# Kernel tuning notes

Measured on AMD Instinct MI355X. Metric: run time of the kernel, lower is better.

The kernel has to match this reference:

```python
import jax, jax.numpy as jnp
import numpy as np

DIMS = 1024
FF_DIMS = 4096
EPS = 1e-5


def _ln(x, g, b):
    m = jnp.mean(x, axis=-1, keepdims=True)
    v = jnp.mean(jnp.square(x - m), axis=-1, keepdims=True)
    return (x - m) * jax.lax.rsqrt(v + EPS) * g + b


def _bind(a, b):
    # HRR bind = circular convolution via FFT
    n = b.shape[-1]
    return jnp.fft.irfft(jnp.fft.rfft(a) * jnp.fft.rfft(b), n=n)


def _unbind(s, a):
    # HRR unbind = circular correlation (bind with approximate inverse) = conj in freq
    n = s.shape[-1]
    return jnp.fft.irfft(jnp.fft.rfft(s) * jnp.conj(jnp.fft.rfft(a)), n=n)


def setup_inputs() -> dict:
    key = jax.random.key(0)
    ks = jax.random.split(key, 16)
    d, f = DIMS, FF_DIMS
    s_d = 1.0 / np.sqrt(d)
    s_f = 1.0 / np.sqrt(f)
    return {
        "x": jax.random.normal(ks[0], (4, 4096, d), jnp.float32),
        "Wq": jax.random.normal(ks[1], (d, d), jnp.float32) * s_d,
        "bq": jnp.zeros((d,), jnp.float32),
        "gq": jnp.ones((d,), jnp.float32),
        "betaq": jnp.zeros((d,), jnp.float32),
        "Wk": jax.random.normal(ks[2], (d, d), jnp.float32) * s_d,
        "bk": jnp.zeros((d,), jnp.float32),
        "gk": jnp.ones((d,), jnp.float32),
        "betak": jnp.zeros((d,), jnp.float32),
        "g0": jnp.ones((d,), jnp.float32),
        "beta0": jnp.zeros((d,), jnp.float32),
        "W1": jax.random.normal(ks[3], (f, d), jnp.float32) * s_d,
        "b1": jnp.zeros((f,), jnp.float32),
        "W2": jax.random.normal(ks[4], (d, f), jnp.float32) * s_f,
        "b2": jnp.zeros((d,), jnp.float32),
        "g1": jnp.ones((d,), jnp.float32),
        "beta1": jnp.zeros((d,), jnp.float32),
    }


def reference(x, Wq, bq, gq, betaq, Wk, bk, gk, betak, g0, beta0,
              W1, b1, W2, b2, g1, beta1):
    # HolographicMixer (dropout is identity in eval)
    q = _ln(jnp.einsum('bse,de->bsd', x, Wq) + bq, gq, betaq)
    k = _ln(jnp.einsum('bse,de->bsd', x, Wk) + bk, gk, betak)
    xb = _bind(k, x)                      # (B,S,D)
    s = jnp.sum(xb, axis=1, keepdims=True)  # (B,1,D)
    vals = _unbind(s, q)                  # broadcast (B,1,D)x(B,S,D)->(B,S,D)
    mix = xb + vals
    x = _ln(x + mix, g0, beta0)
    # FeedForward
    h = jax.nn.relu(jnp.einsum('bsd,fd->bsf', x, W1) + b1)
    ff = jnp.einsum('bsf,df->bsd', h, W2) + b2
    x = _ln(x + ff, g1, beta1)
    return x
```

## Files before the change

kernel.cpp:

```cpp
#include <hip/hip_runtime.h>

typedef unsigned short u16;
typedef unsigned int   u32;
typedef __attribute__((ext_vector_type(8))) __bf16 bf16x8;
typedef __attribute__((ext_vector_type(4))) float   f32x4;

#define NT   16384
#define DD   1024
#define FFD  4096

#define SREG  ((size_t)33554432)
#define S1O   ((size_t)0)
#define S2O   (SREG)
#define S3O   (2*SREG)
#define S4O   (3*SREG)
#define O_WQ  (4*SREG)
#define O_WK  (O_WQ + (size_t)2097152)
#define O_W1  (O_WK + (size_t)2097152)
#define O_W2  (O_W1 + (size_t)8388608)
#define O_FWD (O_W2 + (size_t)8388608)
#define O_INV (O_FWD + (size_t)2097152)
#define O_SF  (O_INV + (size_t)2097152)

__device__ __forceinline__ float b2f(u16 h) {
    u32 u = ((u32)h) << 16;
    return __uint_as_float(u);
}
__device__ __forceinline__ u16 f2b(float f) {
    u32 u = __float_as_uint(f);
    u32 r = (u + 0x7FFFu + ((u >> 16) & 1u)) >> 16;
    return (u16)r;
}

__device__ __forceinline__ void ld16(const u16* g, u16* l) {
    __builtin_amdgcn_global_load_lds(
        (const __attribute__((address_space(1))) void*)g,
        (__attribute__((address_space(3))) void*)l, 16, 0, 0);
}

__device__ __forceinline__ void block_red2(float& a, float& b, float* red, int tid) {
#pragma unroll
    for (int off = 32; off; off >>= 1) {
        a += __shfl_down(a, off, 64);
        b += __shfl_down(b, off, 64);
    }
    int w = tid >> 6;
    if ((tid & 63) == 0) { red[w] = a; red[4 + w] = b; }
    __syncthreads();
    a = red[0] + red[1] + red[2] + red[3];
    b = red[4] + red[5] + red[6] + red[7];
}

__global__ void zero_sf_k(float* __restrict__ Sf) {
    int i = blockIdx.x * 256 + threadIdx.x;
    if (i < 4096) Sf[i] = 0.f;
}

__global__ void cast_f32_bf16_k(const float* __restrict__ s, u16* __restrict__ d, int n4) {
    int i = blockIdx.x * 256 + threadIdx.x;
    if (i < n4) {
        float4 v = ((const float4*)s)[i];
        ushort4 o;
        o.x = f2b(v.x); o.y = f2b(v.y); o.z = f2b(v.z); o.w = f2b(v.w);
        ((ushort4*)d)[i] = o;
    }
}

__global__ void gen_fwd_k(u16* __restrict__ Fwd) {
    int idx = blockIdx.x * 256 + threadIdx.x;
    int n = idx >> 10, k = idx & 1023;
    int f  = (n == 0) ? 0 : ((n & 1) ? ((n + 1) >> 1) : (n >> 1));
    bool re = (n == 0) || (n & 1);
    int r = (f * k) & 1023;
    float ang = (float)r * 6.1359233e-3f;
    float v = re ? __cosf(ang) : -__sinf(ang);
    Fwd[idx] = f2b(v);
}
__global__ void gen_inv_k(u16* __restrict__ Inv) {
    int idx = blockIdx.x * 256 + threadIdx.x;
    int d = idx >> 10, n = idx & 1023;
    int f  = (n == 0) ? 0 : ((n & 1) ? ((n + 1) >> 1) : (n >> 1));
    bool re = (n == 0) || (n & 1);
    int r = (f * d) & 1023;
    float ang = (float)r * 6.1359233e-3f;
    float c = (f == 0 || f == 512) ? (1.0f / 1024.0f) : (2.0f / 1024.0f);
    float v = re ? c * __cosf(ang) : -c * __sinf(ang);
    Inv[idx] = f2b(v);
}

#define BM 256
#define BN 256
#define BK 64
#define EPI_BF16            0
#define EPI_BIAS_BF16       1
#define EPI_BIAS_RELU_BF16  2
#define EPI_BIAS_ADDB_F32   3
#define EPI_ADD_F32         4

#define MFMA16 __builtin_amdgcn_mfma_f32_16x16x32_bf16
#define BARRIER()    asm volatile("s_barrier" ::: "memory")
#define WAIT_LGKM0() asm volatile("s_waitcnt lgkmcnt(0)" ::: "memory")
#define WAIT_VM0()   asm volatile("s_waitcnt vmcnt(0)" ::: "memory")

template <int EPI>
__global__ __launch_bounds__(512, 2) void gemm_bt_k(
    const u16* __restrict__ A, const u16* __restrict__ B, void* __restrict__ Cout,
    const float* __restrict__ bias, const u16* __restrict__ addp16,
    int K, int lda, int ldb, int ldc)
{
    __shared__ __align__(16) u16 As[BM * BK];
    __shared__ __align__(16) u16 Bs[BN * BK];
    const int tid = threadIdx.x;

    int m0, n0;
    {
        const int id = blockIdx.y * gridDim.x + blockIdx.x;
        const int nb = gridDim.x * gridDim.y;
        if ((nb & 7) == 0) {
            const int per = nb >> 3;
            const int t = (id & 7) * per + (id >> 3);
            n0 = (t % gridDim.x) * BN;
            m0 = (t / gridDim.x) * BM;
        } else {
            n0 = blockIdx.x * BN;
            m0 = blockIdx.y * BM;
        }
    }

    const int wid = tid >> 6, l = tid & 63;
    const int wm = (wid >> 2) << 7;
    const int wn = (wid & 3) << 6;
    const int tm = l & 15, quad = l >> 4;
    const int cx0 = ((quad ^ (tm & 7)) << 3);
    const int cx1 = (((quad + 4) ^ (tm & 7)) << 3);

    f32x4 acc[8][4] = {};

    const int srow = tid >> 3;
    const int scol = ((tid & 7) ^ (srow & 7)) << 3;
    const u16* Ag = A + (size_t)(m0 + srow) * lda + scol;
    const u16* Bg = B + (size_t)(n0 + srow) * ldb + scol;
    u16* Asl = As + tid * 8;
    u16* Bsl = Bs + tid * 8;
    const size_t a64 = (size_t)64 * lda, b64 = (size_t)64 * ldb;

    const u16* ArA = As + (wm + tm) * BK;
    const u16* ArB = Bs + (wn + tm) * BK;

    const int ntk = K >> 6;

#pragma unroll
    for (int h = 0; h < 4; ++h) {
        ld16(Ag + (size_t)h * a64, Asl + h * 4096);
        ld16(Bg + (size_t)h * b64, Bsl + h * 4096);
    }
    WAIT_VM0();
    BARRIER();

    for (int t = 0; t < ntk; ++t) {
        const size_t kn = (size_t)(((t + 1 < ntk) ? (t + 1) : t) << 6);
        bf16x8 a[4][2], bA[2][2], bB[2][2];

#pragma unroll
        for (int i = 0; i < 4; ++i) {
            a[i][0] = *(const bf16x8*)(const void*)(ArA + i * 1024 + cx0);
            a[i][1] = *(const bf16x8*)(const void*)(ArA + i * 1024 + cx1);
        }
#pragma unroll
        for (int j = 0; j < 2; ++j) {
            bA[j][0] = *(const bf16x8*)(const void*)(ArB + j * 1024 + cx0);
            bA[j][1] = *(const bf16x8*)(const void*)(ArB + j * 1024 + cx1);
        }
        WAIT_LGKM0();
        __builtin_amdgcn_s_setprio(1);
#pragma unroll
        for (int i = 0; i < 4; ++i)
#pragma unroll
            for (int j = 0; j < 2; ++j) {
                acc[i][j] = MFMA16(a[i][0], bA[j][0], acc[i][j], 0, 0, 0);
                acc[i][j] = MFMA16(a[i][1], bA[j][1], acc[i][j], 0, 0, 0);
            }
        __builtin_amdgcn_s_setprio(0);
        BARRIER();

        ld16(Ag + kn,                 Asl);
        ld16(Ag + kn + 2 * a64,       Asl + 2 * 4096);
#pragma unroll
        for (int j = 0; j < 2; ++j) {
            bB[j][0] = *(const bf16x8*)(const void*)(ArB + (2 + j) * 1024 + cx0);
            bB[j][1] = *(const bf16x8*)(const void*)(ArB + (2 + j) * 1024 + cx1);
        }
        WAIT_LGKM0();
        __builtin_amdgcn_s_setprio(1);
#pragma unroll
        for (int i = 0; i < 4; ++i)
#pragma unroll
            for (int j = 0; j < 2; ++j) {
                acc[i][2 + j] = MFMA16(a[i][0], bB[j][0], acc[i][2 + j], 0, 0, 0);
                acc[i][2 + j] = MFMA16(a[i][1], bB[j][1], acc[i][2 + j], 0, 0, 0);
            }
        __builtin_amdgcn_s_setprio(0);
        BARRIER();

#pragma unroll
        for (int h = 0; h < 4; ++h)
            ld16(Bg + kn + (size_t)h * b64, Bsl + h * 4096);
#pragma unroll
        for (int i = 0; i < 4; ++i) {
            a[i][0] = *(const bf16x8*)(const void*)(ArA + (4 + i) * 1024 + cx0);
            a[i][1] = *(const bf16x8*)(const void*)(ArA + (4 + i) * 1024 + cx1);
        }
        WAIT_LGKM0();
        __builtin_amdgcn_s_setprio(1);
#pragma unroll
        for (int i = 0; i < 4; ++i)
#pragma unroll
            for (int j = 0; j < 2; ++j) {
                acc[4 + i][2 + j] = MFMA16(a[i][0], bB[j][0], acc[4 + i][2 + j], 0, 0, 0);
                acc[4 + i][2 + j] = MFMA16(a[i][1], bB[j][1], acc[4 + i][2 + j], 0, 0, 0);
            }
        __builtin_amdgcn_s_setprio(0);
        BARRIER();

        ld16(Ag + kn + a64,           Asl + 4096);
        ld16(Ag + kn + 3 * a64,       Asl + 3 * 4096);
        __builtin_amdgcn_s_setprio(1);
#pragma unroll
        for (int i = 0; i < 4; ++i)
#pragma unroll
            for (int j = 0; j < 2; ++j) {
                acc[4 + i][j] = MFMA16(a[i][0], bA[j][0], acc[4 + i][j], 0, 0, 0);
                acc[4 + i][j] = MFMA16(a[i][1], bA[j][1], acc[4 + i][j], 0, 0, 0);
            }
        __builtin_amdgcn_s_setprio(0);
        WAIT_VM0();
        BARRIER();
    }

#pragma unroll
    for (int i = 0; i < 8; ++i) {
        const int gmb = m0 + wm + i * 16 + (quad << 2);
#pragma unroll
        for (int j = 0; j < 4; ++j) {
            const int gn = n0 + wn + j * 16 + tm;
            float bv = 0.f;
            if (EPI == EPI_BIAS_BF16 || EPI == EPI_BIAS_RELU_BF16 || EPI == EPI_BIAS_ADDB_F32)
                bv = bias[gn];
#pragma unroll
            for (int r = 0; r < 4; ++r) {
                size_t off = (size_t)(gmb + r) * ldc + gn;
                float v = acc[i][j][r] + bv;
                if (EPI == EPI_BIAS_ADDB_F32) v += b2f(addp16[off]);
                if (EPI == EPI_ADD_F32)       v += ((const float*)Cout)[off];
                if (EPI == EPI_BIAS_RELU_BF16) v = fmaxf(v, 0.f);
                if (EPI == EPI_BF16 || EPI == EPI_BIAS_BF16 || EPI == EPI_BIAS_RELU_BF16)
                    ((u16*)Cout)[off] = f2b(v);
                else
                    ((float*)Cout)[off] = v;
            }
        }
    }
}

__global__ void ln_bf16_k(const u16* __restrict__ src, u16* __restrict__ dst,
                          const float* __restrict__ g, const float* __restrict__ be) {
    __shared__ float red[8];
    const int t = blockIdx.x, tid = threadIdx.x;
    ushort4 h = ((const ushort4*)(src + (size_t)t * DD))[tid];
    float4 v = { b2f(h.x), b2f(h.y), b2f(h.z), b2f(h.w) };
    float s  = v.x + v.y + v.z + v.w;
    float ss = v.x * v.x + v.y * v.y + v.z * v.z + v.w * v.w;
    block_red2(s, ss, red, tid);
    float mean = s * (1.f / 1024.f);
    float inv  = 1.0f / sqrtf(ss * (1.f / 1024.f) - mean * mean + 1e-5f);
    float4 gv = ((const float4*)g)[tid];
    float4 bv = ((const float4*)be)[tid];
    ushort4 o;
    o.x = f2b((v.x - mean) * inv * gv.x + bv.x);
    o.y = f2b((v.y - mean) * inv * gv.y + bv.y);
    o.z = f2b((v.z - mean) * inv * gv.z + bv.z);
    o.w = f2b((v.w - mean) * inv * gv.w + bv.w);
    ((ushort4*)(dst + (size_t)t * DD))[tid] = o;
}

__global__ void ln_out_k(float* __restrict__ io, const float* __restrict__ g,
                         const float* __restrict__ be) {
    __shared__ float red[8];
    const int t = blockIdx.x, tid = threadIdx.x;
    float4 v = ((const float4*)(io + (size_t)t * DD))[tid];
    float s  = v.x + v.y + v.z + v.w;
    float ss = v.x * v.x + v.y * v.y + v.z * v.z + v.w * v.w;
    block_red2(s, ss, red, tid);
    float mean = s * (1.f / 1024.f);
    float inv  = 1.0f / sqrtf(ss * (1.f / 1024.f) - mean * mean + 1e-5f);
    float4 gv = ((const float4*)g)[tid];
    float4 bv = ((const float4*)be)[tid];
    float4 o;
    o.x = (v.x - mean) * inv * gv.x + bv.x;
    o.y = (v.y - mean) * inv * gv.y + bv.y;
    o.z = (v.z - mean) * inv * gv.z + bv.z;
    o.w = (v.w - mean) * inv * gv.w + bv.w;
    ((float4*)(io + (size_t)t * DD))[tid] = o;
}

#define PW1_TOK 16
__global__ void pw1_k(const u16* __restrict__ FTx, const u16* __restrict__ FTk,
                      float* __restrict__ Sf) {
    const int tid = threadIdx.x;
    const int t0 = blockIdx.x * PW1_TOK;
    const int b = t0 >> 12;
    float a0 = 0.f;
    float ar1 = 0.f, ai1 = 0.f;
    float ar2 = 0.f, ai2 = 0.f;
    const int f1 = tid + 1, f2 = tid + 257;
    for (int it = 0; it < PW1_TOK; ++it) {
        const size_t ro = (size_t)(t0 + it) * DD;
        const u16* rx = FTx + ro;
        const u16* rk = FTk + ro;
        if (tid == 0) a0 += b2f(rk[0]) * b2f(rx[0]);
        {
            float xr = b2f(rx[2 * f1 - 1]), xi = b2f(rx[2 * f1]);
            float kr = b2f(rk[2 * f1 - 1]), ki = b2f(rk[2 * f1]);
            ar1 += kr * xr - ki * xi;
            ai1 += kr * xi + ki * xr;
        }
        if (f2 < 512) {
            float xr = b2f(rx[2 * f2 - 1]), xi = b2f(rx[2 * f2]);
            float kr = b2f(rk[2 * f2 - 1]), ki = b2f(rk[2 * f2]);
            ar2 += kr * xr - ki * xi;
            ai2 += kr * xi + ki * xr;
        } else {
            ar2 += b2f(rk[1023]) * b2f(rx[1023]);
        }
    }
    float* sb = Sf + (size_t)b * DD;
    if (tid == 0) atomicAdd(&sb[0], a0);
    atomicAdd(&sb[2 * f1 - 1], ar1);
    atomicAdd(&sb[2 * f1],     ai1);
    if (f2 < 512) {
        atomicAdd(&sb[2 * f2 - 1], ar2);
        atomicAdd(&sb[2 * f2],     ai2);
    } else {
        atomicAdd(&sb[1023], ar2);
    }
}

__global__ void pw2_k(u16* __restrict__ FTx, const u16* __restrict__ FTk,
                      const u16* __restrict__ FTq, const float* __restrict__ Sf) {
    const int t = blockIdx.x, tid = threadIdx.x;
    const int b = t >> 12;
    const size_t ro = (size_t)t * DD;
    u16* rx = FTx + ro;
    const u16* rk = FTk + ro;
    const u16* rq = FTq + ro;
    const float* sb = Sf + (size_t)b * DD;
    const int f1 = tid + 1, f2 = tid + 257;
    if (tid == 0) {
        float x = b2f(rx[0]), k = b2f(rk[0]), q = b2f(rq[0]);
        rx[0] = f2b(x + k * x + sb[0] * q);
    }
    {
        float xr = b2f(rx[2 * f1 - 1]), xi = b2f(rx[2 * f1]);
        float kr = b2f(rk[2 * f1 - 1]), ki = b2f(rk[2 * f1]);
        float qr = b2f(rq[2 * f1 - 1]), qi = b2f(rq[2 * f1]);
        float sr = sb[2 * f1 - 1], si = sb[2 * f1];
        rx[2 * f1 - 1] = f2b(xr + (kr * xr - ki * xi) + (sr * qr + si * qi));
        rx[2 * f1]     = f2b(xi + (kr * xi + ki * xr) + (si * qr - sr * qi));
    }
    if (f2 < 512) {
        float xr = b2f(rx[2 * f2 - 1]), xi = b2f(rx[2 * f2]);
        float kr = b2f(rk[2 * f2 - 1]), ki = b2f(rk[2 * f2]);
        float qr = b2f(rq[2 * f2 - 1]), qi = b2f(rq[2 * f2]);
        float sr = sb[2 * f2 - 1], si = sb[2 * f2];
        rx[2 * f2 - 1] = f2b(xr + (kr * xr - ki * xi) + (sr * qr + si * qi));
        rx[2 * f2]     = f2b(xi + (kr * xi + ki * xr) + (si * qr - sr * qi));
    } else {
        float x = b2f(rx[1023]), k = b2f(rk[1023]), q = b2f(rq[1023]);
        rx[1023] = f2b(x + k * x + sb[1023] * q);
    }
}

extern "C" void kernel_launch(void* const* d_in, const int* in_sizes, int n_in,
                              void* d_out, int out_size, void* d_ws, size_t ws_size,
                              hipStream_t stream) {
    const float* x     = (const float*)d_in[0];
    const float* Wq    = (const float*)d_in[1];
    const float* bq    = (const float*)d_in[2];
    const float* gq    = (const float*)d_in[3];
    const float* betaq = (const float*)d_in[4];
    const float* Wk    = (const float*)d_in[5];
    const float* bk    = (const float*)d_in[6];
    const float* gk    = (const float*)d_in[7];
    const float* betak = (const float*)d_in[8];
    const float* g0    = (const float*)d_in[9];
    const float* beta0 = (const float*)d_in[10];
    const float* W1    = (const float*)d_in[11];
    const float* b1    = (const float*)d_in[12];
    const float* W2    = (const float*)d_in[13];
    const float* b2    = (const float*)d_in[14];
    const float* g1    = (const float*)d_in[15];
    const float* beta1 = (const float*)d_in[16];

    char* ws = (char*)d_ws;
    u16* S1 = (u16*)(ws + S1O);
    u16* S2 = (u16*)(ws + S2O);
    u16* S3 = (u16*)(ws + S3O);
    u16* S4 = (u16*)(ws + S4O);
    u16* wq16 = (u16*)(ws + O_WQ);
    u16* wk16 = (u16*)(ws + O_WK);
    u16* w116 = (u16*)(ws + O_W1);
    u16* w216 = (u16*)(ws + O_W2);
    u16* fwdP = (u16*)(ws + O_FWD);
    u16* invP = (u16*)(ws + O_INV);
    float* Sf = (float*)(ws + O_SF);
    float* out = (float*)d_out;

    zero_sf_k<<<16, 256, 0, stream>>>(Sf);
    cast_f32_bf16_k<<<16384, 256, 0, stream>>>(x, S1, 4194304);
    cast_f32_bf16_k<<<1024, 256, 0, stream>>>(Wq, wq16, 262144);
    cast_f32_bf16_k<<<1024, 256, 0, stream>>>(Wk, wk16, 262144);
    cast_f32_bf16_k<<<4096, 256, 0, stream>>>(W1, w116, 1048576);
    cast_f32_bf16_k<<<4096, 256, 0, stream>>>(W2, w216, 1048576);
    gen_fwd_k<<<4096, 256, 0, stream>>>(fwdP);
    gen_inv_k<<<4096, 256, 0, stream>>>(invP);

    gemm_bt_k<EPI_BIAS_BF16><<<dim3(4, 64), 512, 0, stream>>>(S1, wq16, S2, bq, nullptr, 1024, 1024, 1024, 1024);
    gemm_bt_k<EPI_BIAS_BF16><<<dim3(4, 64), 512, 0, stream>>>(S1, wk16, S3, bk, nullptr, 1024, 1024, 1024, 1024);
    ln_bf16_k<<<NT, 256, 0, stream>>>(S2, S2, gq, betaq);
    ln_bf16_k<<<NT, 256, 0, stream>>>(S3, S3, gk, betak);

    gemm_bt_k<EPI_BF16><<<dim3(4, 64), 512, 0, stream>>>(S1, fwdP, S4, nullptr, nullptr, 1024, 1024, 1024, 1024);
    gemm_bt_k<EPI_BF16><<<dim3(4, 64), 512, 0, stream>>>(S3, fwdP, S1, nullptr, nullptr, 1024, 1024, 1024, 1024);
    gemm_bt_k<EPI_BF16><<<dim3(4, 64), 512, 0, stream>>>(S2, fwdP, S3, nullptr, nullptr, 1024, 1024, 1024, 1024);

    pw1_k<<<NT / PW1_TOK, 256, 0, stream>>>(S4, S1, Sf);
    pw2_k<<<NT, 256, 0, stream>>>(S4, S1, S3, Sf);

    gemm_bt_k<EPI_BF16><<<dim3(4, 64), 512, 0, stream>>>(S4, invP, S2, nullptr, nullptr, 1024, 1024, 1024, 1024);

    ln_bf16_k<<<NT, 256, 0, stream>>>(S2, S1, g0, beta0);

    gemm_bt_k<EPI_BIAS_RELU_BF16><<<dim3(8, 64), 512, 0, stream>>>(S1, w116, S3, b1, nullptr, 1024, 1024, 1024, 2048);
    gemm_bt_k<EPI_BIAS_ADDB_F32><<<dim3(4, 64), 512, 0, stream>>>(S3, w216, out, b2, S1, 2048, 2048, 4096, 1024);
    gemm_bt_k<EPI_BIAS_RELU_BF16><<<dim3(8, 64), 512, 0, stream>>>(S1, w116 + (size_t)2048 * 1024, S3, b1 + 2048, nullptr, 1024, 1024, 1024, 2048);
    gemm_bt_k<EPI_ADD_F32><<<dim3(4, 64), 512, 0, stream>>>(S3, w216 + 2048, out, nullptr, nullptr, 2048, 2048, 4096, 1024);

    ln_out_k<<<NT, 256, 0, stream>>>(out, g1, beta1);

    (void)in_sizes; (void)n_in; (void)out_size; (void)ws_size;
}
```

Baseline: 878.6 us.

## Double-buffer GEMM LDS tiles with staggered A/B prefetch and partial vmcnt waits

Converts the bf16 GEMM's single LDS stage into double buffers. A is prefetched one k-step ahead and B two k-steps ahead, and the loop waits on vmcnt(4) instead of draining every load each iteration. The aim is to keep global loads in flight across iterations so MFMA work hides memory latency. In exchange LDS use doubles to 128 KB per block, which may limit occupancy under launch_bounds(512,2), and extra barriers are added around the staging points.

```diff
diff --git a/kernel.cpp b/kernel.cpp
--- a/kernel.cpp
+++ b/kernel.cpp
@@ -90,7 +90,6 @@
 
 #define BM 256
 #define BN 256
-#define BK 64
 #define EPI_BF16            0
 #define EPI_BIAS_BF16       1
 #define EPI_BIAS_RELU_BF16  2
@@ -100,7 +99,17 @@
 #define MFMA16 __builtin_amdgcn_mfma_f32_16x16x32_bf16
 #define BARRIER()    asm volatile("s_barrier" ::: "memory")
 #define WAIT_LGKM0() asm volatile("s_waitcnt lgkmcnt(0)" ::: "memory")
+#define WAIT_VM4()   asm volatile("s_waitcnt vmcnt(4)" ::: "memory")
 #define WAIT_VM0()   asm volatile("s_waitcnt vmcnt(0)" ::: "memory")
+
+#define STAGE_A(k0, b, h) do { \
+    ld16(Ag + (size_t)(k0) + (size_t)(h) * a128,       Asl + (b) * 16384 + (h) * 8192); \
+    ld16(Ag + (size_t)(k0) + (size_t)(h) * a128 + a64, Asl + (b) * 16384 + (h) * 8192 + 4096); \
+} while (0)
+#define STAGE_B(k0, b, h) do { \
+    ld16(Bg + (size_t)(k0) + (size_t)(h) * b128,       Bsl + (b) * 16384 + (h) * 8192); \
+    ld16(Bg + (size_t)(k0) + (size_t)(h) * b128 + b64, Bsl + (b) * 16384 + (h) * 8192 + 4096); \
+} while (0)
 
 template <int EPI>
 __global__ __launch_bounds__(512, 2) void gemm_bt_k(
@@ -108,8 +117,8 @@
     const float* __restrict__ bias, const u16* __restrict__ addp16,
     int K, int lda, int ldb, int ldc)
 {
-    __shared__ __align__(16) u16 As[BM * BK];
-    __shared__ __align__(16) u16 Bs[BN * BK];
+    __shared__ __align__(16) u16 As[2 * BM * 64];
+    __shared__ __align__(16) u16 Bs[2 * BN * 64];
     const int tid = threadIdx.x;
 
     int m0, n0;
@@ -128,11 +137,11 @@
     }
 
     const int wid = tid >> 6, l = tid & 63;
-    const int wm = (wid >> 2) << 7;
-    const int wn = (wid & 3) << 6;
+    const int wm2 = (wid >> 2) << 7;
+    const int wn4 = (wid & 3) << 6;
     const int tm = l & 15, quad = l >> 4;
     const int cx0 = ((quad ^ (tm & 7)) << 3);
-    const int cx1 = (((quad + 4) ^ (tm & 7)) << 3);
+    const int cx1 = cx0 ^ 32;
 
     f32x4 acc[8][4] = {};
 
@@ -143,106 +152,112 @@
     u16* Asl = As + tid * 8;
     u16* Bsl = Bs + tid * 8;
     const size_t a64 = (size_t)64 * lda, b64 = (size_t)64 * ldb;
-
-    const u16* ArA = As + (wm + tm) * BK;
-    const u16* ArB = Bs + (wn + tm) * BK;
+    const size_t a128 = (size_t)128 * lda, b128 = (size_t)128 * ldb;
+
+    const u16* Abase = As + (wm2 + tm) * 64;
+    const u16* Bbase = Bs + (wn4 + tm) * 64;
 
     const int ntk = K >> 6;
 
-#pragma unroll
-    for (int h = 0; h < 4; ++h) {
-        ld16(Ag + (size_t)h * a64, Asl + h * 4096);
-        ld16(Bg + (size_t)h * b64, Bsl + h * 4096);
-    }
-    WAIT_VM0();
+    STAGE_A(0, 0, 0); STAGE_A(0, 0, 1);
+    STAGE_B(0, 0, 0); STAGE_B(0, 0, 1);
+    STAGE_B(64, 1, 0); STAGE_B(64, 1, 1);
+    WAIT_VM4();
     BARRIER();
 
     for (int t = 0; t < ntk; ++t) {
-        const size_t kn = (size_t)(((t + 1 < ntk) ? (t + 1) : t) << 6);
-        bf16x8 a[4][2], bA[2][2], bB[2][2];
+        const int buf = t & 1;
+        const int kA = ((t + 1 < ntk) ? (t + 1) : (ntk - 1)) << 6;
+        const int kB = ((t + 2 < ntk) ? (t + 2) : (ntk - 1)) << 6;
+        const u16* Ab = Abase + buf * 16384;
+        const u16* Bb = Bbase + buf * 16384;
+
+        bf16x8 a03[4][2], a47[4][2], b01[2][2], b23[2][2];
 
 #pragma unroll
         for (int i = 0; i < 4; ++i) {
-            a[i][0] = *(const bf16x8*)(const void*)(ArA + i * 1024 + cx0);
-            a[i][1] = *(const bf16x8*)(const void*)(ArA + i * 1024 + cx1);
+            a03[i][0] = *(const bf16x8*)(const void*)(Ab + i * 1024 + cx0);
+            a03[i][1] = *(const bf16x8*)(const void*)(Ab + i * 1024 + cx1);
         }
 #pragma unroll
         for (int j = 0; j < 2; ++j) {
-            bA[j][0] = *(const bf16x8*)(const void*)(ArB + j * 1024 + cx0);
-            bA[j][1] = *(const bf16x8*)(const void*)(ArB + j * 1024 + cx1);
-        }
+            b01[j][0] = *(const bf16x8*)(const void*)(Bb + j * 1024 + cx0);
+            b01[j][1] = *(const bf16x8*)(const void*)(Bb + j * 1024 + cx1);
+        }
+        STAGE_A(kA, buf ^ 1, 0);
+        BARRIER();
         WAIT_LGKM0();
         __builtin_amdgcn_s_setprio(1);
 #pragma unroll
         for (int i = 0; i < 4; ++i)
 #pragma unroll
             for (int j = 0; j < 2; ++j) {
-                acc[i][j] = MFMA16(a[i][0], bA[j][0], acc[i][j], 0, 0, 0);
-                acc[i][j] = MFMA16(a[i][1], bA[j][1], acc[i][j], 0, 0, 0);
+                acc[i][j] = MFMA16(a03[i][0], b01[j][0], acc[i][j], 0, 0, 0);
+                acc[i][j] = MFMA16(a03[i][1], b01[j][1], acc[i][j], 0, 0, 0);
             }
         __builtin_amdgcn_s_setprio(0);
         BARRIER();
 
-        ld16(Ag + kn,                 Asl);
-        ld16(Ag + kn + 2 * a64,       Asl + 2 * 4096);
 #pragma unroll
         for (int j = 0; j < 2; ++j) {
-            bB[j][0] = *(const bf16x8*)(const void*)(ArB + (2 + j) * 1024 + cx0);
-            bB[j][1] = *(const bf16x8*)(const void*)(ArB + (2 + j) * 1024 + cx1);
-        }
+            b23[j][0] = *(const bf16x8*)(const void*)(Bb + (2 + j) * 1024 + cx0);
+            b23[j][1] = *(const bf16x8*)(const void*)(Bb + (2 + j) * 1024 + cx1);
+        }
+        STAGE_A(kA, buf ^ 1, 1);
+        BARRIER();
         WAIT_LGKM0();
         __builtin_amdgcn_s_setprio(1);
 #pragma unroll
         for (int i = 0; i < 4; ++i)
 #pragma unroll
             for (int j = 0; j < 2; ++j) {
-                acc[i][2 + j] = MFMA16(a[i][0], bB[j][0], acc[i][2 + j], 0, 0, 0);
-                acc[i][2 + j] = MFMA16(a[i][1], bB[j][1], acc[i][2 + j], 0, 0, 0);
+                acc[i][2 + j] = MFMA16(a03[i][0], b23[j][0], acc[i][2 + j], 0, 0, 0);
+                acc[i][2 + j] = MFMA16(a03[i][1], b23[j][1], acc[i][2 + j], 0, 0, 0);
             }
         __builtin_amdgcn_s_setprio(0);
         BARRIER();
 
 #pragma unroll
-        for (int h = 0; h < 4; ++h)
-            ld16(Bg + kn + (size_t)h * b64, Bsl + h * 4096);
-#pragma unroll
         for (int i = 0; i < 4; ++i) {
-            a[i][0] = *(const bf16x8*)(const void*)(ArA + (4 + i) * 1024 + cx0);
-            a[i][1] = *(const bf16x8*)(const void*)(ArA + (4 + i) * 1024 + cx1);
-        }
+            a47[i][0] = *(const bf16x8*)(const void*)(Ab + (4 + i) * 1024 + cx0);
+            a47[i][1] = *(const bf16x8*)(const void*)(Ab + (4 + i) * 1024 + cx1);
+        }
+        STAGE_B(kB, buf, 0);
+        BARRIER();
         WAIT_LGKM0();
         __builtin_amdgcn_s_setprio(1);
 #pragma unroll
         for (int i = 0; i < 4; ++i)
 #pragma unroll
             for (int j = 0; j < 2; ++j) {
-                acc[4 + i][2 + j] = MFMA16(a[i][0], bB[j][0], acc[4 + i][2 + j], 0, 0, 0);
-                acc[4 + i][2 + j] = MFMA16(a[i][1], bB[j][1], acc[4 + i][2 + j], 0, 0, 0);
+                acc[4 + i][2 + j] = MFMA16(a47[i][0], b23[j][0], acc[4 + i][2 + j], 0, 0, 0);
+                acc[4 + i][2 + j] = MFMA16(a47[i][1], b23[j][1], acc[4 + i][2 + j], 0, 0, 0);
             }
         __builtin_amdgcn_s_setprio(0);
         BARRIER();
 
-        ld16(Ag + kn + a64,           Asl + 4096);
-        ld16(Ag + kn + 3 * a64,       Asl + 3 * 4096);
+        STAGE_B(kB, buf, 1);
+        BARRIER();
         __builtin_amdgcn_s_setprio(1);
 #pragma unroll
         for (int i = 0; i < 4; ++i)
 #pragma unroll
             for (int j = 0; j < 2; ++j) {
-                acc[4 + i][j] = MFMA16(a[i][0], bA[j][0], acc[4 + i][j], 0, 0, 0);
-                acc[4 + i][j] = MFMA16(a[i][1], bA[j][1], acc[4 + i][j], 0, 0, 0);
+                acc[4 + i][j] = MFMA16(a47[i][0], b01[j][0], acc[4 + i][j], 0, 0, 0);
+                acc[4 + i][j] = MFMA16(a47[i][1], b01[j][1], acc[4 + i][j], 0, 0, 0);
             }
         __builtin_amdgcn_s_setprio(0);
-        WAIT_VM0();
-        BARRIER();
-    }
+        WAIT_VM4();
+        BARRIER();
+    }
+    WAIT_VM0();
 
 #pragma unroll
     for (int i = 0; i < 8; ++i) {
-        const int gmb = m0 + wm + i * 16 + (quad << 2);
+        const int gmb = m0 + wm2 + i * 16 + (quad << 2);
 #pragma unroll
         for (int j = 0; j < 4; ++j) {
-            const int gn = n0 + wn + j * 16 + tm;
+            const int gn = n0 + wn4 + j * 16 + tm;
             float bv = 0.f;
             if (EPI == EPI_BIAS_BF16 || EPI == EPI_BIAS_RELU_BF16 || EPI == EPI_BIAS_ADDB_F32)
                 bv = bias[gn];
```

Measured after the change: 854.4 us. 2.8% less time.
